# Optimization experiments

Measured on AMD Instinct MI355X. Metric: run time of the kernel, lower is better.

## Reference

```python
import jax, jax.numpy as jnp
import numpy as np

N = 100000      # nodes
E = 1600000     # edges
F_IN = 256      # input features
H = 128         # hidden_dim
C = 40          # num_classes
L = 4           # num_layers
STEP = 0.1


def setup_inputs() -> dict:
    key = jax.random.key(0)
    ks = jax.random.split(key, 8)
    s = 0.05
    return {
        "x": jax.random.normal(ks[0], (N, F_IN), jnp.float32),
        "edge_index": jax.random.randint(ks[1], (2, E), 0, N),
        "enc_W": jax.random.normal(ks[2], (H, F_IN), jnp.float32) * s,
        "enc_b": jnp.zeros((H,), jnp.float32),
        "W_raw": jax.random.normal(ks[3], (L, H, H + 2), jnp.float32) * s,
        "W_b": jnp.zeros((L, H), jnp.float32),
        "ext_w": jax.random.normal(ks[4], (L, H), jnp.float32),
        "beta": jax.random.normal(ks[5], (L,), jnp.float32),
        "dec_W": jax.random.normal(ks[6], (C, H), jnp.float32) * s,
        "dec_b": jnp.zeros((C,), jnp.float32),
    }


def _pairwise_weight(Wr):
    # Wr: (H, H+2) raw weight -> symmetric effective weight (H, H)
    W0 = jnp.triu(Wr[:, :-2], 1)
    W0 = W0 + W0.T
    diag = Wr[:, -2] * jnp.sum(jnp.abs(W0), axis=1) + Wr[:, -1]
    return W0 + jnp.diag(diag)


def reference(x, edge_index, enc_W, enc_b, W_raw, W_b, ext_w, beta, dec_W, dec_b):
    row, col = edge_index[0], edge_index[1]
    n = x.shape[0]
    # degree over source nodes (edge_index[0]), recomputed identically each layer
    deg = jnp.zeros((n,), x.dtype).at[row].add(jnp.float32(1.0))
    deg_inv = jnp.where(deg > 0, jnp.where(deg > 0, deg, 1.0) ** -0.5, 0.0)
    # message = deg_inv[row]*deg_inv[col] * x_i (x_i = features of target col),
    # scatter-added at target col  ==>  per-node coefficient times node feature
    coef = jnp.zeros((n,), x.dtype).at[col].add(deg_inv[row] * deg_inv[col])

    h = x @ enc_W.T + enc_b
    h0 = h
    for l in range(W_raw.shape[0]):
        W_eff = _pairwise_weight(W_raw[l])        # symmetric (H,H)
        out_p = h @ W_eff.T + W_b[l]              # pairwise linear transform
        agg = coef[:, None] * out_p               # gather+normalize+scatter-add
        out = agg - (h * ext_w[l][None, :] + beta[l] * h0)
        h = h + STEP * jax.nn.relu(out)
    return h @ dec_W.T + dec_b
```

## Files before the change

### kernel.cpp

```cpp
#include <hip/hip_runtime.h>

typedef unsigned int u32;
typedef unsigned short u16;
typedef __bf16 bf16x8 __attribute__((ext_vector_type(8)));
typedef float f32x16 __attribute__((ext_vector_type(16)));
typedef u32 u32x4 __attribute__((ext_vector_type(4)));

#define HDIM 128
#define FIN  256
#define NCLS 40
#define NL   4
#define BN   16384
#define NSL  32

__device__ __forceinline__ u16 f2b(float f){
  union { __bf16 h; u16 s; } u; u.h = (__bf16)f; return u.s;
}
__device__ __forceinline__ u32 pk(float a, float b){
  union { __bf16 h[2]; u32 w; } u; u.h[0] = (__bf16)a; u.h[1] = (__bf16)b; return u.w;
}
__device__ __forceinline__ float ubf(u32 hbits){
  union { u32 w; float f; } u; u.w = hbits << 16; return u.f;
}
__device__ __forceinline__ float dinv(float d){ return d > 0.f ? rsqrtf(d) : 0.f; }

__device__ __forceinline__ int fragIdx128(int row, int k){
  return (((((row >> 5) * 8 + (k >> 4)) * 2 + ((k >> 3) & 1)) * 32 + (row & 31)) * 8) + (k & 7);
}
__device__ __forceinline__ int fragIdx64(int row, int k){
  return (((((row >> 5) * 4 + (k >> 4)) * 2 + ((k >> 3) & 1)) * 32 + (row & 31)) * 8) + (k & 7);
}

__device__ __forceinline__ void stage16k_async(u16* lds, const u16* src, int wv, int lane){
  #pragma unroll
  for(int i = 0; i < 4; i++){
    const int off = (wv * 4 + i) * 1024;
    __builtin_amdgcn_global_load_lds(
      (const __attribute__((address_space(1))) void*)((const char*)src + off + lane * 16),
      (__attribute__((address_space(3))) void*)((char*)lds + off),
      16, 0, 0);
  }
}

__device__ __forceinline__ void stage32k_async(u16* lds, const u16* src, int wv, int lane){
  #pragma unroll
  for(int i = 0; i < 8; i++){
    const int off = (wv * 8 + i) * 1024;
    __builtin_amdgcn_global_load_lds(
      (const __attribute__((address_space(1))) void*)((const char*)src + off + lane * 16),
      (__attribute__((address_space(3))) void*)((char*)lds + off),
      16, 0, 0);
  }
}

__global__ void prep_kernel(const float* __restrict__ encW, const float* __restrict__ Wraw,
                            const float* __restrict__ decW,
                            u16* __restrict__ encF, u16* __restrict__ weffF, u16* __restrict__ decB){
  int b = blockIdx.x, t = threadIdx.x;
  if(b < 512){
    int i = b * 64 + t;
    int row = i >> 8, k = i & 255;
    int chunk = k >> 6, kk = k & 63;
    encF[chunk * 8192 + fragIdx64(row, kk)] = f2b(encW[i]);
  } else if(b < 1024){
    int idx = b - 512;
    int l = idx >> 7, i = idx & 127;
    const float* Wr = Wraw + (size_t)l * HDIM * (HDIM + 2);
    float w0a, w0b, s = 0.f;
    { int j = t;
      float v = (i < j) ? Wr[i*(HDIM+2)+j] : ((j < i) ? Wr[j*(HDIM+2)+i] : 0.f);
      w0a = v; s += fabsf(v); }
    { int j = t + 64;
      float v = (i < j) ? Wr[i*(HDIM+2)+j] : ((j < i) ? Wr[j*(HDIM+2)+i] : 0.f);
      w0b = v; s += fabsf(v); }
    #pragma unroll
    for(int d = 1; d < 64; d <<= 1) s += __shfl_xor(s, d, 64);
    float diag = Wr[i*(HDIM+2)+HDIM] * s + Wr[i*(HDIM+2)+HDIM+1];
    u16* o = weffF + (size_t)l * 16384;
    o[fragIdx128(i, t)]      = f2b((t == i)      ? diag : w0a);
    o[fragIdx128(i, t + 64)] = f2b((t + 64 == i) ? diag : w0b);
  } else {
    int idx = b - 1024;
    int i = idx * 64 + t;
    int c = i >> 7, k = i & 127;
    decB[i] = (c < NCLS) ? f2b(decW[c * HDIM + k]) : (u16)0;
  }
}


template<int WEIGHTED>
__device__ void hist_body(float* buck, int b, int tid,
                          const int* __restrict__ idx, const int* __restrict__ src,
                          const float* __restrict__ dv, float* __restrict__ partial,
                          int E, int Nn, int NB, int chunk)
{
  const int g = b % NB;
  const int s = b / NB;
  const int lo = g << 14;

  for(int i = tid; i < BN; i += 256) buck[i] = 0.f;
  __syncthreads();

  long e0 = (long)s * chunk;
  long e1 = (long)E < e0 + chunk ? (long)E : e0 + chunk;
  if(e0 < e1){
    long ng = (e1 - e0) >> 2;
    for(long gi = tid; gi < ng; gi += 256){
      long e = e0 + gi * 4;
      int4 c = *(const int4*)(idx + e);
      int4 r;
      if(WEIGHTED) r = *(const int4*)(src + e);
      int k;
      k = c.x - lo; if((u32)k < (u32)BN) atomicAdd(&buck[k], WEIGHTED ? dv[r.x] : 1.f);
      k = c.y - lo; if((u32)k < (u32)BN) atomicAdd(&buck[k], WEIGHTED ? dv[r.y] : 1.f);
      k = c.z - lo; if((u32)k < (u32)BN) atomicAdd(&buck[k], WEIGHTED ? dv[r.z] : 1.f);
      k = c.w - lo; if((u32)k < (u32)BN) atomicAdd(&buck[k], WEIGHTED ? dv[r.w] : 1.f);
    }
    long et = e0 + ng * 4;
    if(et + tid < e1){
      long e = et + tid;
      int k = idx[e] - lo;
      if((u32)k < (u32)BN) atomicAdd(&buck[k], WEIGHTED ? dv[src[e]] : 1.f);
    }
  }
  __syncthreads();

  float* dst = partial + (size_t)s * ((size_t)NB << 14) + lo;
  int hi = Nn - lo < BN ? Nn - lo : BN;
  for(int i = tid; i < hi; i += 256) dst[i] = buck[i];
}

template<int WEIGHTED>
__global__ void __launch_bounds__(256, 2)
hist_kernel(const int* __restrict__ idx, const int* __restrict__ src,
            const float* __restrict__ dv, float* __restrict__ partial,
            int E, int Nn, int NB, int chunk)
{
  __shared__ float buck[BN];
  hist_body<WEIGHTED>(buck, blockIdx.x, threadIdx.x, idx, src, dv, partial, E, Nn, NB, chunk);
}

template<int MODE>
__global__ void reduce_kernel(const float* __restrict__ partial, const float* __restrict__ dvin,
                              float* __restrict__ outv, int Nn, int NB, int S)
{
  int i = blockIdx.x * 256 + threadIdx.x;
  if(i >= Nn) return;
  const size_t NnPad = (size_t)NB << 14;
  float t = 0.f;
  for(int s = 0; s < S; s++) t += partial[(size_t)s * NnPad + i];
  outv[i] = MODE ? dvin[i] * t : (t > 0.f ? rsqrtf(t) : 0.f);
}


__global__ void deg_kernel(const int* __restrict__ ei, float* __restrict__ deg, int E){
  long e = ((long)blockIdx.x * 256 + threadIdx.x) * 8;
  if(e + 7 < E){
    int4 v0 = *(const int4*)(ei + e);
    int4 v1 = *(const int4*)(ei + e + 4);
    atomicAdd(&deg[v0.x], 1.0f); atomicAdd(&deg[v0.y], 1.0f);
    atomicAdd(&deg[v0.z], 1.0f); atomicAdd(&deg[v0.w], 1.0f);
    atomicAdd(&deg[v1.x], 1.0f); atomicAdd(&deg[v1.y], 1.0f);
    atomicAdd(&deg[v1.z], 1.0f); atomicAdd(&deg[v1.w], 1.0f);
  } else {
    for(; e < E; e++) atomicAdd(&deg[ei[e]], 1.0f);
  }
}

__global__ void coef_kernel(const int* __restrict__ ei, const float* __restrict__ deg,
                            float* __restrict__ coef, int E){
  long e = ((long)blockIdx.x * 256 + threadIdx.x) * 8;
  if(e + 7 < E){
    int4 r0 = *(const int4*)(ei + e);
    int4 r1 = *(const int4*)(ei + e + 4);
    int4 c0 = *(const int4*)(ei + E + e);
    int4 c1 = *(const int4*)(ei + E + e + 4);
    atomicAdd(&coef[c0.x], dinv(deg[r0.x]) * dinv(deg[c0.x]));
    atomicAdd(&coef[c0.y], dinv(deg[r0.y]) * dinv(deg[c0.y]));
    atomicAdd(&coef[c0.z], dinv(deg[r0.z]) * dinv(deg[c0.z]));
    atomicAdd(&coef[c0.w], dinv(deg[r0.w]) * dinv(deg[c0.w]));
    atomicAdd(&coef[c1.x], dinv(deg[r1.x]) * dinv(deg[c1.x]));
    atomicAdd(&coef[c1.y], dinv(deg[r1.y]) * dinv(deg[c1.y]));
    atomicAdd(&coef[c1.z], dinv(deg[r1.z]) * dinv(deg[c1.z]));
    atomicAdd(&coef[c1.w], dinv(deg[r1.w]) * dinv(deg[c1.w]));
  } else {
    for(; e < E; e++){
      int r = ei[e], c = ei[E + e];
      atomicAdd(&coef[c], dinv(deg[r]) * dinv(deg[c]));
    }
  }
}

__device__ __forceinline__ bf16x8 buildBp(u32 P0, u32 P1, u32 P2, u32 P3, int hi){
  u32 S0 = hi ? P0 : P2;
  u32 S1 = hi ? P1 : P3;
  u32 R0 = __shfl_xor(S0, 32, 64);
  u32 R1 = __shfl_xor(S1, 32, 64);
  union { u32 w[4]; bf16x8 b; } u;
  u.w[0] = hi ? R0 : P0;
  u.w[1] = hi ? R1 : P1;
  u.w[2] = hi ? P2 : R0;
  u.w[3] = hi ? P3 : R1;
  return u.b;
}

__device__ void enc_body(u16* lw, u16* xc, int blk, int tid,
                         const float* __restrict__ x, const float* __restrict__ enc_b,
                         const u16* __restrict__ encF, u32* __restrict__ h0F, int Nn)
{
  const int lane = tid & 63;
  const int wv   = tid >> 6;
  const int hi   = lane >> 5;
  const int ln   = lane & 31;
  const int nib  = wv * 32 + ln;

  f32x16 acc[4];
  #pragma unroll
  for(int nt = 0; nt < 4; nt++)
    #pragma unroll
    for(int i = 0; i < 16; i++) acc[nt][i] = 0.f;

  const int r0 = tid >> 4;
  const int c4 = (tid & 15) * 4;
  const int g  = c4 >> 3, j = c4 & 7;

  for(int chunk = 0; chunk < 4; chunk++){
    __syncthreads();
    stage16k_async(lw, encF + chunk * 8192, wv, lane);
    #pragma unroll
    for(int i = 0; i < 8; i++){
      int r = i * 16 + r0;
      int gn = blk * 128 + r; if(gn >= Nn) gn = Nn - 1;
      float4 v = *(const float4*)(x + (size_t)gn * FIN + chunk * 64 + c4);
      u32* d = (u32*)(xc + g * 1024 + ((r ^ (g & 7)) << 3) + j);
      d[0] = pk(v.x, v.y);
      d[1] = pk(v.z, v.w);
    }
    __syncthreads();

    #pragma unroll
    for(int ksl = 0; ksl < 4; ksl++){
      #pragma unroll
      for(int nt = 0; nt < 4; nt++){
        const int gg = ksl * 2 + hi;
        const bf16x8 B = *(const bf16x8*)(xc + gg * 1024 + ((nib ^ (gg & 7)) << 3));
        const bf16x8 A = *(const bf16x8*)(lw + ((((nt * 4 + ksl) * 2 + hi) * 32 + ln) * 8));
        acc[nt] = __builtin_amdgcn_mfma_f32_32x32x16_bf16(A, B, acc[nt], 0, 0, 0);
      }
    }
  }

  u32* dst = h0F + (size_t)blk * 8192;
  #pragma unroll
  for(int nt = 0; nt < 4; nt++){
    #pragma unroll
    for(int q = 0; q < 4; q++){
      float4 eb = *(const float4*)(enc_b + nt * 32 + 8 * q + 4 * hi);
      acc[nt][4*q+0] += eb.x; acc[nt][4*q+1] += eb.y;
      acc[nt][4*q+2] += eb.z; acc[nt][4*q+3] += eb.w;
    }
    #pragma unroll
    for(int m = 0; m < 8; m++)
      dst[(nt * 8 + m) * 256 + tid] = pk(acc[nt][2*m], acc[nt][2*m+1]);
  }
}

__global__ void __launch_bounds__(256, 2)
enc_kernel(const float* __restrict__ x, const float* __restrict__ enc_b,
           const u16* __restrict__ encF, u32* __restrict__ h0F, int Nn)
{
  __shared__ u16 lw[8192];
  __shared__ u16 xc[8192];
  enc_body(lw, xc, blockIdx.x, threadIdx.x, x, enc_b, encF, h0F, Nn);
}

__global__ void __launch_bounds__(256, 2)
kA_kernel(const int* __restrict__ ei, float* __restrict__ partial,
          int E, int Nn, int NB, int chunk, int nbHist,
          const float* __restrict__ x, const float* __restrict__ enc_b,
          const u16* __restrict__ encF, u32* __restrict__ h0F)
{
  __shared__ __align__(16) char smem[65536];
  const int b = blockIdx.x, tid = threadIdx.x;
  if(b < nbHist){
    hist_body<0>((float*)smem, b, tid, ei, ei, (const float*)nullptr, partial, E, Nn, NB, chunk);
  } else {
    enc_body((u16*)smem, (u16*)(smem + 16384), b - nbHist, tid, x, enc_b, encF, h0F, Nn);
  }
}

__global__ void __launch_bounds__(256, 2)
lay_kernel(const float* __restrict__ W_b, const float* __restrict__ ext_w,
           const float* __restrict__ beta, const float* __restrict__ dec_b,
           const float* __restrict__ coef, const u32* __restrict__ h0F,
           const u16* __restrict__ weffF, const u16* __restrict__ decB,
           float* __restrict__ out, int Nn)
{
  __shared__ u16 lw[16384];
  __shared__ u32 hns[16][256];

  const int tid  = threadIdx.x;
  const int lane = tid & 63;
  const int wv   = tid >> 6;
  const int hi   = lane >> 5;
  const int ln   = lane & 31;
  const int nib  = wv * 32 + ln;
  const int node = blockIdx.x * 128 + nib;
  const int nd   = node < Nn ? node : (Nn - 1);
  const float cf = coef[nd];

  u32 hp[32];
  const u32* srcH = h0F + (size_t)blockIdx.x * 8192;
  #pragma unroll
  for(int m = 0; m < 32; m++)
    hp[m] = srcH[m * 256 + tid];

  for(int l = 0; l < NL; l++){
    __syncthreads();
    stage32k_async(lw, weffF + l * 16384, wv, lane);
    __syncthreads();

    const float bet = beta[l];

    #pragma unroll
    for(int P = 0; P < 2; P++){
      f32x16 a0, a1;
      #pragma unroll
      for(int i = 0; i < 16; i++){ a0[i] = 0.f; a1[i] = 0.f; }

      #pragma unroll
      for(int ks = 0; ks < 8; ks++){
        const int wbase = (ks >> 1) * 8 + 4 * (ks & 1);
        bf16x8 B = buildBp(hp[wbase+0], hp[wbase+1], hp[wbase+2], hp[wbase+3], hi);
        const bf16x8 A0 = *(const bf16x8*)(lw + (((((2*P+0) * 8 + ks) * 2 + hi) * 32 + ln) * 8));
        const bf16x8 A1 = *(const bf16x8*)(lw + (((((2*P+1) * 8 + ks) * 2 + hi) * 32 + ln) * 8));
        a0 = __builtin_amdgcn_mfma_f32_32x32x16_bf16(A0, B, a0, 0, 0, 0);
        a1 = __builtin_amdgcn_mfma_f32_32x32x16_bf16(A1, B, a1, 0, 0, 0);
      }

      #pragma unroll
      for(int t = 0; t < 2; t++){
        const int nt = 2*P + t;
        f32x16& a = t ? a1 : a0;
        #pragma unroll
        for(int q = 0; q < 4; q++){
          const int fb = nt * 32 + 8 * q + 4 * hi;
          float4 wb = *(const float4*)(W_b   + l * HDIM + fb);
          float4 ew = *(const float4*)(ext_w + l * HDIM + fb);
          #pragma unroll
          for(int r2 = 0; r2 < 4; r2++){
            const int r = 4 * q + r2;
            float wbv = (r2==0)?wb.x:(r2==1)?wb.y:(r2==2)?wb.z:wb.w;
            float ewv = (r2==0)?ew.x:(r2==1)?ew.y:(r2==2)?ew.z:ew.w;
            u32 w0 = srcH[(nt * 8 + (r >> 1)) * 256 + tid];
            u32 wc = hp[nt * 8 + (r >> 1)];
            float h0v = ubf((r & 1) ? (w0 >> 16) : (w0 & 0xffffu));
            float hv  = ubf((r & 1) ? (wc >> 16) : (wc & 0xffffu));
            float o = cf * (a[r] + wbv) - hv * ewv - bet * h0v;
            a[r] = hv + 0.1f * fmaxf(o, 0.f);
          }
        }
        #pragma unroll
        for(int m = 0; m < 8; m++){
          u32 w = pk(a[2*m], a[2*m+1]);
          if(P == 0) hns[nt * 8 + m][tid] = w;
          else       hp[nt * 8 + m] = w;
        }
      }
    }
    #pragma unroll
    for(int m = 0; m < 16; m++) hp[m] = hns[m][tid];
  }

  f32x16 d0, d1;
  #pragma unroll
  for(int i = 0; i < 16; i++){ d0[i] = 0.f; d1[i] = 0.f; }

  #pragma unroll
  for(int ks = 0; ks < 8; ks++){
    const int wbase = (ks >> 1) * 8 + 4 * (ks & 1);
    bf16x8 B = buildBp(hp[wbase+0], hp[wbase+1], hp[wbase+2], hp[wbase+3], hi);
    const bf16x8 A0 = *(const bf16x8*)(decB + (0 * 32 + ln) * HDIM + ks * 16 + hi * 8);
    const bf16x8 A1 = *(const bf16x8*)(decB + (1 * 32 + ln) * HDIM + ks * 16 + hi * 8);
    d0 = __builtin_amdgcn_mfma_f32_32x32x16_bf16(A0, B, d0, 0, 0, 0);
    d1 = __builtin_amdgcn_mfma_f32_32x32x16_bf16(A1, B, d1, 0, 0, 0);
  }

  if(node < Nn){
    #pragma unroll
    for(int nt = 0; nt < 2; nt++){
      const f32x16& d = nt ? d1 : d0;
      #pragma unroll
      for(int q = 0; q < 4; q++){
        if(nt == 0 || q == 0){
          const int c0 = nt * 32 + 8 * q + 4 * hi;
          float4 db = *(const float4*)(dec_b + c0);
          float4 v;
          v.x = d[4*q+0] + db.x;
          v.y = d[4*q+1] + db.y;
          v.z = d[4*q+2] + db.z;
          v.w = d[4*q+3] + db.w;
          *(float4*)(out + (size_t)node * NCLS + c0) = v;
        }
      }
    }
  }
}

extern "C" void kernel_launch(void* const* d_in, const int* in_sizes, int n_in,
                              void* d_out, int out_size, void* d_ws, size_t ws_size,
                              hipStream_t stream){
  (void)n_in; (void)out_size;
  const float* x     = (const float*)d_in[0];
  const int*   ei    = (const int*)  d_in[1];
  const float* encW  = (const float*)d_in[2];
  const float* enc_b = (const float*)d_in[3];
  const float* Wraw  = (const float*)d_in[4];
  const float* W_b   = (const float*)d_in[5];
  const float* ext_w = (const float*)d_in[6];
  const float* beta  = (const float*)d_in[7];
  const float* decW  = (const float*)d_in[8];
  const float* dec_b = (const float*)d_in[9];
  float* out = (float*)d_out;
  const int Nn = in_sizes[0] / FIN;
  const int E  = in_sizes[1] / 2;
  const int nBlk = (Nn + 127) / 128;
  const int NB   = (Nn + BN - 1) / BN;
  const int chunk = (((E + NSL - 1) / NSL) + 3) & ~3;
  const int nbHist = NB * NSL;

  char* ws = (char*)d_ws;
  size_t szN = ((size_t)Nn * 4 + 511) & ~(size_t)511;
  float* coef = (float*)(ws);
  float* dv   = (float*)(ws + szN);
  u16* encF   = (u16*)(ws + 2 * szN);
  u16* weffF  = (u16*)(ws + 2 * szN + 65536);
  u16* decB   = (u16*)(ws + 2 * szN + 65536 + 131072);
  u32* h0F    = (u32*)(ws + 2 * szN + 65536 + 131072 + 16384);
  float* partial = (float*)(ws + 2 * szN + 65536 + 131072 + 16384 + (size_t)nBlk * 32768);
  const size_t partialBytes = (size_t)NSL * ((size_t)NB << 14) * 4;
  const size_t need = 2 * szN + 65536 + 131072 + 16384 + (size_t)nBlk * 32768 + partialBytes;
  const bool fast = ws_size >= need;

  prep_kernel<<<1152, 64, 0, stream>>>(encW, Wraw, decW, encF, weffF, decB);
  const int ngrid = (Nn + 255) / 256;
  if(fast){
    kA_kernel<<<nbHist + nBlk, 256, 0, stream>>>(ei, partial, E, Nn, NB, chunk, nbHist,
                                                 x, enc_b, encF, h0F);
    reduce_kernel<0><<<ngrid, 256, 0, stream>>>(partial, dv, dv, Nn, NB, NSL);
    hist_kernel<1><<<nbHist, 256, 0, stream>>>(ei + E, ei, dv, partial, E, Nn, NB, chunk);
    reduce_kernel<1><<<ngrid, 256, 0, stream>>>(partial, dv, coef, Nn, NB, NSL);
  } else {
    const int egrid = (int)((E / 8 + 255) / 256) + 1;
    hipMemsetAsync(ws, 0, 2 * szN, stream);
    deg_kernel <<<egrid, 256, 0, stream>>>(ei, dv, E);
    coef_kernel<<<egrid, 256, 0, stream>>>(ei, dv, coef, E);
    enc_kernel <<<nBlk, 256, 0, stream>>>(x, enc_b, encF, h0F, Nn);
  }
  lay_kernel <<<nBlk, 256, 0, stream>>>(W_b, ext_w, beta, dec_b, coef, h0F, weffF, decB, out, Nn);
}
```

Baseline: 176.5 us.

## Fuse encoder with second histogram pass and inline coef reduction into layer kernel

```diff
diff --git a/kernel.cpp b/kernel.cpp
--- a/kernel.cpp
+++ b/kernel.cpp
@@ -275,24 +275,27 @@
 }
 
 __global__ void __launch_bounds__(256, 2)
-kA_kernel(const int* __restrict__ ei, float* __restrict__ partial,
-          int E, int Nn, int NB, int chunk, int nbHist,
+kB_kernel(const int* __restrict__ ei, const float* __restrict__ dv, float* __restrict__ partial,
+          int E, int Nn, int NB, int chunk, int nEnc,
           const float* __restrict__ x, const float* __restrict__ enc_b,
           const u16* __restrict__ encF, u32* __restrict__ h0F)
 {
   __shared__ __align__(16) char smem[65536];
   const int b = blockIdx.x, tid = threadIdx.x;
-  if(b < nbHist){
-    hist_body<0>((float*)smem, b, tid, ei, ei, (const float*)nullptr, partial, E, Nn, NB, chunk);
-  } else {
-    enc_body((u16*)smem, (u16*)(smem + 16384), b - nbHist, tid, x, enc_b, encF, h0F, Nn);
-  }
-}
-
+  if(b < nEnc){
+    enc_body((u16*)smem, (u16*)(smem + 16384), b, tid, x, enc_b, encF, h0F, Nn);
+  } else {
+    hist_body<1>((float*)smem, b - nEnc, tid, ei + E, ei, dv, partial, E, Nn, NB, chunk);
+  }
+}
+
+template<bool INLC>
 __global__ void __launch_bounds__(256, 2)
 lay_kernel(const float* __restrict__ W_b, const float* __restrict__ ext_w,
            const float* __restrict__ beta, const float* __restrict__ dec_b,
-           const float* __restrict__ coef, const u32* __restrict__ h0F,
+           const float* __restrict__ coef, const float* __restrict__ dv,
+           const float* __restrict__ partial, int NB,
+           const u32* __restrict__ h0F,
            const u16* __restrict__ weffF, const u16* __restrict__ decB,
            float* __restrict__ out, int Nn)
 {
@@ -307,7 +310,17 @@
   const int nib  = wv * 32 + ln;
   const int node = blockIdx.x * 128 + nib;
   const int nd   = node < Nn ? node : (Nn - 1);
-  const float cf = coef[nd];
+
+  float cf;
+  if(INLC){
+    const size_t NnPad = (size_t)NB << 14;
+    float s = 0.f;
+    #pragma unroll 4
+    for(int sl = 0; sl < NSL; sl++) s += partial[(size_t)sl * NnPad + nd];
+    cf = dv[nd] * s;
+  } else {
+    cf = coef[nd];
+  }
 
   u32 hp[32];
   const u32* srcH = h0F + (size_t)blockIdx.x * 8192;
@@ -445,17 +458,19 @@
   prep_kernel<<<1152, 64, 0, stream>>>(encW, Wraw, decW, encF, weffF, decB);
   const int ngrid = (Nn + 255) / 256;
   if(fast){
-    kA_kernel<<<nbHist + nBlk, 256, 0, stream>>>(ei, partial, E, Nn, NB, chunk, nbHist,
+    hist_kernel<0><<<nbHist, 256, 0, stream>>>(ei, ei, dv, partial, E, Nn, NB, chunk);
+    reduce_kernel<0><<<ngrid, 256, 0, stream>>>(partial, dv, dv, Nn, NB, NSL);
+    kB_kernel<<<nBlk + nbHist, 256, 0, stream>>>(ei, dv, partial, E, Nn, NB, chunk, nBlk,
                                                  x, enc_b, encF, h0F);
-    reduce_kernel<0><<<ngrid, 256, 0, stream>>>(partial, dv, dv, Nn, NB, NSL);
-    hist_kernel<1><<<nbHist, 256, 0, stream>>>(ei + E, ei, dv, partial, E, Nn, NB, chunk);
-    reduce_kernel<1><<<ngrid, 256, 0, stream>>>(partial, dv, coef, Nn, NB, NSL);
+    lay_kernel<true><<<nBlk, 256, 0, stream>>>(W_b, ext_w, beta, dec_b, coef, dv, partial, NB,
+                                               h0F, weffF, decB, out, Nn);
   } else {
     const int egrid = (int)((E / 8 + 255) / 256) + 1;
     hipMemsetAsync(ws, 0, 2 * szN, stream);
     deg_kernel <<<egrid, 256, 0, stream>>>(ei, dv, E);
     coef_kernel<<<egrid, 256, 0, stream>>>(ei, dv, coef, E);
     enc_kernel <<<nBlk, 256, 0, stream>>>(x, enc_b, encF, h0F, Nn);
-  }
-  lay_kernel <<<nBlk, 256, 0, stream>>>(W_b, ext_w, beta, dec_b, coef, h0F, weffF, decB, out, Nn);
-}
+    lay_kernel<false><<<nBlk, 256, 0, stream>>>(W_b, ext_w, beta, dec_b, coef, dv, partial, NB,
+                                                h0F, weffF, decB, out, Nn);
+  }
+}
```

After: 178.3 us. About the same (+1.0%).
